# Optimization experiments

Hardware: AMD Instinct MI355X
Metric: run time of the kernel (lower is better)

Reference implementation:

```python
import jax, jax.numpy as jnp
import numpy as np

B, S, D, U = 64, 1024, 512, 512  # batch, seq_len, input dim, lstm units


def setup_inputs() -> dict:
    key = jax.random.key(0)
    ks = jax.random.split(key, 8)
    inputs = jax.random.normal(ks[0], (B, S, D), dtype=jnp.float32)
    # padded speech batch: valid prefix lengths in [S//2, S]
    lengths = jax.random.randint(ks[1], (B,), S // 2, S + 1)
    mask = jnp.arange(S)[None, :] < lengths[:, None]  # [B, S] bool
    s_in, s_rec = 1.0 / np.sqrt(D), 1.0 / np.sqrt(U)
    # Keras LSTM params per direction: kernel [D,4U], recurrent_kernel [U,4U], bias [4U]
    # gate order i, f, g(cell), o ; unit_forget_bias -> forget-gate bias = 1
    bias0 = jnp.zeros((4 * U,), jnp.float32).at[U:2 * U].set(1.0)
    return {
        "inputs": inputs,
        "mask": mask,
        "kernel_f": jax.random.normal(ks[2], (D, 4 * U), jnp.float32) * s_in,
        "rkernel_f": jax.random.normal(ks[3], (U, 4 * U), jnp.float32) * s_rec,
        "bias_f": bias0,
        "kernel_b": jax.random.normal(ks[4], (D, 4 * U), jnp.float32) * s_in,
        "rkernel_b": jax.random.normal(ks[5], (U, 4 * U), jnp.float32) * s_rec,
        "bias_b": bias0,
    }


def _masked_lstm(x, mask, kernel, rkernel, bias):
    """Keras-semantics masked LSTM. x:[B,S,D], mask:[B,S] -> (hs:[B,S,U], h:[B,U], c:[B,U]).
    Masked timesteps carry previous h/c (and emit previous h)."""
    units = rkernel.shape[0]
    # precompute input projection once (big GEMM)
    xz = jnp.einsum('bsd,dk->bsk', x, kernel) + bias  # [B,S,4U]

    def step(carry, inp):
        h, c = carry
        zx, m = inp  # zx:[B,4U], m:[B]
        z = zx + h @ rkernel
        i, f, g, o = jnp.split(z, 4, axis=-1)
        c_new = jax.nn.sigmoid(f) * c + jax.nn.sigmoid(i) * jnp.tanh(g)
        h_new = jax.nn.sigmoid(o) * jnp.tanh(c_new)
        m = m[:, None]
        h = jnp.where(m, h_new, h)
        c = jnp.where(m, c_new, c)
        return (h, c), h

    h0 = jnp.zeros((x.shape[0], units), x.dtype)
    (h, c), hs = jax.lax.scan(step, (h0, h0),
                              (jnp.swapaxes(xz, 0, 1), jnp.swapaxes(mask, 0, 1)))
    return jnp.swapaxes(hs, 0, 1), h, c


def reference(inputs, mask, kernel_f, rkernel_f, bias_f, kernel_b, rkernel_b, bias_b):
    # forward direction
    fwd_out, h_f, c_f = _masked_lstm(inputs, mask, kernel_f, rkernel_f, bias_f)
    # go_backwards=True: Keras reverses inputs AND mask along time
    bwd_out, h_b, c_b = _masked_lstm(inputs[:, ::-1], mask[:, ::-1], kernel_b, rkernel_b, bias_b)
    # wrapper: concat(forward, reverse(backward)) along features
    output = jnp.concatenate([fwd_out, bwd_out[:, ::-1]], axis=-1)  # [B,S,2U]
    return output, h_f, c_f, h_b, c_b
```

## Files before the change

### kernel.cpp

```cpp
#include <hip/hip_runtime.h>

#define S_LEN 1024
#define B_SZ  64
#define D_IN  512
#define U_SZ  512
#define NWG_DIR 64
#define UNITS_PER_WG 8
#define NT 2
#define KSTEPS 32

typedef __attribute__((ext_vector_type(8))) short short8;
typedef __attribute__((ext_vector_type(4))) float floatx4;

union HQ { unsigned long long q[2]; short8 s; };

__device__ __forceinline__ unsigned short f2bf(float f) {
  union { float f; unsigned u; } v; v.f = f;
  unsigned r = v.u + 0x7fffu + ((v.u >> 16) & 1u);
  return (unsigned short)(r >> 16);
}
__device__ __forceinline__ float fsig(float x) {
  return __builtin_amdgcn_rcpf(1.0f + __expf(-x));
}
__device__ __forceinline__ float ftanh(float x) {
  return 1.0f - 2.0f * __builtin_amdgcn_rcpf(__expf(2.0f * x) + 1.0f);
}

__global__ void xprep_kernel(const float* __restrict__ x,
                             unsigned short* __restrict__ Axt) {
  int bs = blockIdx.x;
  int b = bs >> 10, s = bs & 1023;
  float4 v = ((const float4*)x)[(size_t)bs * 128 + threadIdx.x];
  ushort4 o;
  o.x = f2bf(v.x); o.y = f2bf(v.y); o.z = f2bf(v.z); o.w = f2bf(v.w);
  ((ushort4*)(Axt + ((size_t)s * B_SZ + b) * D_IN))[threadIdx.x] = o;
}

__global__ void maskpack_kernel(const unsigned int* __restrict__ mraw,
                                unsigned long long* __restrict__ maskbits) {
  int t = blockIdx.x * blockDim.x + threadIdx.x;
  if (t >= S_LEN) return;
  unsigned d0 = mraw[0];
  unsigned long long bits = 0;
  if (d0 == 1u) {
    const int* m = (const int*)mraw;
    for (int b = 0; b < B_SZ; ++b) if (m[b * S_LEN + t]) bits |= 1ull << b;
  } else if (d0 == 0x3f800000u) {
    const float* m = (const float*)mraw;
    for (int b = 0; b < B_SZ; ++b) if (m[b * S_LEN + t] != 0.f) bits |= 1ull << b;
  } else {
    const unsigned char* m = (const unsigned char*)mraw;
    for (int b = 0; b < B_SZ; ++b) if (m[b * S_LEN + t]) bits |= 1ull << b;
  }
  maskbits[t] = bits;
}

__global__ __launch_bounds__(256, 1) void lstm_scan_kernel(
    const unsigned short* __restrict__ Axt,
    const float* __restrict__ kernel_f, const float* __restrict__ rkernel_f,
    const float* __restrict__ bias_f,
    const float* __restrict__ kernel_b, const float* __restrict__ rkernel_b,
    const float* __restrict__ bias_b,
    const unsigned long long* __restrict__ maskbits,
    unsigned short* __restrict__ hbuf,
    unsigned int* __restrict__ ctrs,
    float* __restrict__ out) {
  __shared__ alignas(16) short lds_b[NT * KSTEPS * 64 * 8];

  const int tid  = threadIdx.x;
  const int lane = tid & 63;
  const int wv   = tid >> 6;
  const int dir  = blockIdx.x >> 6;
  const int wg   = blockIdx.x & 63;
  const int u0   = wg * UNITS_PER_WG;

  const float* Wk   = dir ? kernel_b  : kernel_f;
  const float* Rk   = dir ? rkernel_b : rkernel_f;
  const float* bias = dir ? bias_b    : bias_f;

  for (int item = tid; item < NT * KSTEPS * 64; item += 256) {
    int nt = item >> 11;
    int rem = item & 2047;
    int ks = rem >> 6;
    int ln = rem & 63;
    int kbase = ks * 32 + ((ln >> 4) << 3);
    int col16 = ln & 15;
    int gate = nt * 2 + (col16 >> 3);
    int cg = gate * U_SZ + u0 + (col16 & 7);
    short8 v;
#pragma unroll
    for (int j = 0; j < 8; ++j) {
      int k = kbase + j;
      float f = (k < D_IN) ? Wk[(size_t)k * 2048 + cg]
                           : Rk[(size_t)(k - D_IN) * 2048 + cg];
      v[j] = (short)f2bf(f);
    }
    *(short8*)(&lds_b[item * 8]) = v;
  }
  __syncthreads();

  const int du = lane & 7;
  const int u  = u0 + du;
  float bz[4];
#pragma unroll
  for (int g = 0; g < 4; ++g) bz[g] = bias[g * U_SZ + u];

  float c_st[4] = {0.f, 0.f, 0.f, 0.f};
  float h_st[4] = {0.f, 0.f, 0.f, 0.f};

  unsigned short* hb_base = hbuf + (size_t)dir * 2 * B_SZ * U_SZ;
  unsigned int* ctr = ctrs + dir * 64;

  const int mrow  = lane & 15;
  const int kq    = (lane >> 4) << 3;
  const bool active = (lane & 8) == 0;
  const int brow0 = wv * 16 + ((lane >> 4) << 2);
  const int brow  = wv * 16 + mrow;

  for (int t = 0; t < S_LEN; ++t) {
    const int sx = dir ? (S_LEN - 1 - t) : t;
    const unsigned short* xs =
        Axt + (size_t)sx * B_SZ * D_IN + (size_t)brow * D_IN + kq;
    floatx4 acc0 = {0.f, 0.f, 0.f, 0.f};
    floatx4 acc1 = {0.f, 0.f, 0.f, 0.f};

#pragma unroll
    for (int ks = 0; ks < 16; ++ks) {
      short8 a  = *(const short8*)(xs + ks * 32);
      short8 b0 = *(const short8*)(&lds_b[((0 * KSTEPS + ks) * 64 + lane) * 8]);
      short8 b1 = *(const short8*)(&lds_b[((1 * KSTEPS + ks) * 64 + lane) * 8]);
      acc0 = __builtin_amdgcn_mfma_f32_16x16x32_bf16(a, b0, acc0, 0, 0, 0);
      acc1 = __builtin_amdgcn_mfma_f32_16x16x32_bf16(a, b1, acc1, 0, 0, 0);
    }

    const unsigned long long mb = maskbits[sx];

    if (t > 0) {
      if (tid == 0) {
        unsigned target = (unsigned)(NWG_DIR * t);
        while (__hip_atomic_load(ctr, __ATOMIC_RELAXED,
                                 __HIP_MEMORY_SCOPE_AGENT) < target)
          __builtin_amdgcn_s_sleep(1);
      }
      __syncthreads();
    }

    const unsigned long long* hr = (const unsigned long long*)(
        hb_base + (size_t)((t + 1) & 1) * B_SZ * U_SZ);
    HQ hq[16];
#pragma unroll
    for (int ks = 0; ks < 16; ++ks) {
      int wgp = ks * 4 + (lane >> 4);
      const unsigned long long* p = hr + (size_t)(wgp * 64 + brow) * 2;
      hq[ks].q[0] = __hip_atomic_load(p, __ATOMIC_RELAXED,
                                      __HIP_MEMORY_SCOPE_AGENT);
      hq[ks].q[1] = __hip_atomic_load(p + 1, __ATOMIC_RELAXED,
                                      __HIP_MEMORY_SCOPE_AGENT);
    }
#pragma unroll
    for (int ks = 0; ks < 16; ++ks) {
      short8 b0 = *(const short8*)(&lds_b[((0 * KSTEPS + 16 + ks) * 64 + lane) * 8]);
      short8 b1 = *(const short8*)(&lds_b[((1 * KSTEPS + 16 + ks) * 64 + lane) * 8]);
      acc0 = __builtin_amdgcn_mfma_f32_16x16x32_bf16(hq[ks].s, b0, acc0, 0, 0, 0);
      acc1 = __builtin_amdgcn_mfma_f32_16x16x32_bf16(hq[ks].s, b1, acc1, 0, 0, 0);
    }

#pragma unroll
    for (int r = 0; r < 4; ++r) {
      float iv = acc0[r];
      float gv = acc1[r];
      float fv = __shfl_xor(iv, 8, 64);
      float ov = __shfl_xor(gv, 8, 64);
      float zi = iv + bz[0], zf = fv + bz[1], zg = gv + bz[2], zo = ov + bz[3];
      float cn = fsig(zf) * c_st[r] + fsig(zi) * ftanh(zg);
      float hn = fsig(zo) * ftanh(cn);
      int b = brow0 + r;
      bool m = (mb >> b) & 1ull;
      c_st[r] = m ? cn : c_st[r];
      h_st[r] = m ? hn : h_st[r];
    }

    {
      unsigned short* hw = hb_base + (size_t)(t & 1) * B_SZ * U_SZ +
                           (size_t)wg * 512;
#pragma unroll
      for (int r = 0; r < 4; ++r) {
        unsigned hv = f2bf(h_st[r]);
        unsigned pv = (unsigned)__shfl_xor((int)hv, 1, 64);
        unsigned packed = (hv & 0xffffu) | (pv << 16);
        if (active && !(lane & 1)) {
          int b = brow0 + r;
          __hip_atomic_store((unsigned*)(hw + b * 8 + du), packed,
                             __ATOMIC_RELAXED, __HIP_MEMORY_SCOPE_AGENT);
        }
      }
    }

    asm volatile("s_waitcnt vmcnt(0)" ::: "memory");
    __syncthreads();
    if (tid == 0)
      __hip_atomic_fetch_add(ctr, 1u, __ATOMIC_RELAXED,
                             __HIP_MEMORY_SCOPE_AGENT);

    if (active) {
#pragma unroll
      for (int r = 0; r < 4; ++r) {
        int b = brow0 + r;
        __builtin_nontemporal_store(
            h_st[r], out + ((size_t)b * S_LEN + sx) * 1024 + dir * U_SZ + u);
      }
      if (t == S_LEN - 1) {
        float* fin = out + (size_t)B_SZ * S_LEN * 1024 +
                     (size_t)dir * 2 * B_SZ * U_SZ;
#pragma unroll
        for (int r = 0; r < 4; ++r) {
          int b = brow0 + r;
          fin[b * U_SZ + u] = h_st[r];
          fin[B_SZ * U_SZ + b * U_SZ + u] = c_st[r];
        }
      }
    }
  }
}

extern "C" void kernel_launch(void* const* d_in, const int* in_sizes, int n_in,
                              void* d_out, int out_size, void* d_ws, size_t ws_size,
                              hipStream_t stream) {
  const float* inputs    = (const float*)d_in[0];
  const void*  mask      = d_in[1];
  const float* kernel_f  = (const float*)d_in[2];
  const float* rkernel_f = (const float*)d_in[3];
  const float* bias_f    = (const float*)d_in[4];
  const float* kernel_b  = (const float*)d_in[5];
  const float* rkernel_b = (const float*)d_in[6];
  const float* bias_b    = (const float*)d_in[7];
  float* out = (float*)d_out;

  char* ws = (char*)d_ws;
  unsigned short* Axt = (unsigned short*)ws;
  size_t off = (size_t)S_LEN * B_SZ * D_IN * 2;
  unsigned short* hbuf = (unsigned short*)(ws + off);
  unsigned int* ctrs = (unsigned int*)(ws + off + 262144);
  unsigned long long* maskbits =
      (unsigned long long*)(ws + off + 262144 + 512);

  hipMemsetAsync(hbuf, 0, 262144 + 512, stream);
  maskpack_kernel<<<4, 256, 0, stream>>>((const unsigned int*)mask, maskbits);
  xprep_kernel<<<S_LEN * B_SZ, 128, 0, stream>>>(inputs, Axt);
  lstm_scan_kernel<<<128, 256, 0, stream>>>(Axt, kernel_f, rkernel_f, bias_f,
                                            kernel_b, rkernel_b, bias_b,
                                            maskbits, hbuf, ctrs, out);
}
```

Measured before the change: 6.116 ms.

## Partition LSTM scan by XCD with batch groups and per-slot flag sync

Measured after the change: 4.968 ms. -18.8%, faster.

```diff
diff --git a/kernel.cpp b/kernel.cpp
--- a/kernel.cpp
+++ b/kernel.cpp
@@ -4,15 +4,13 @@
 #define B_SZ  64
 #define D_IN  512
 #define U_SZ  512
-#define NWG_DIR 64
-#define UNITS_PER_WG 8
-#define NT 2
-#define KSTEPS 32
+#define SPIN_CAP (1 << 20)
 
 typedef __attribute__((ext_vector_type(8))) short short8;
 typedef __attribute__((ext_vector_type(4))) float floatx4;
-
-union HQ { unsigned long long q[2]; short8 s; };
+typedef __attribute__((ext_vector_type(4))) unsigned uintx4;
+
+union HU { uintx4 u; short8 s; };
 
 __device__ __forceinline__ unsigned short f2bf(float f) {
   union { float f; unsigned u; } v; v.f = f;
@@ -55,170 +53,184 @@
   maskbits[t] = bits;
 }
 
+__global__ void wprep_kernel(const float* __restrict__ kf,
+                             const float* __restrict__ rf,
+                             const float* __restrict__ kb,
+                             const float* __restrict__ rb,
+                             unsigned short* __restrict__ Wt) {
+  int item = blockIdx.x * 256 + threadIdx.x;
+  int c   = item & 2047;
+  int kc  = (item >> 11) & 255;
+  int dir = item >> 19;
+  const float* K = dir ? kb : kf;
+  const float* R = dir ? rb : rf;
+  int k0 = kc * 4;
+  unsigned long long pk = 0;
+#pragma unroll
+  for (int i = 0; i < 4; ++i) {
+    int k = k0 + i;
+    float f = (k < D_IN) ? K[(size_t)k * 2048 + c]
+                         : R[(size_t)(k - D_IN) * 2048 + c];
+    pk |= (unsigned long long)f2bf(f) << (16 * i);
+  }
+  *(unsigned long long*)(Wt + ((size_t)dir * 2048 + c) * 1024 + k0) = pk;
+}
+
+#define HLOAD(k, boff) \
+  asm volatile("global_load_dwordx4 %0, %1, off offset:" #boff " sc0" \
+               : "=v"(hq[k].u) : "v"(hr))
+
 __global__ __launch_bounds__(256, 1) void lstm_scan_kernel(
     const unsigned short* __restrict__ Axt,
-    const float* __restrict__ kernel_f, const float* __restrict__ rkernel_f,
-    const float* __restrict__ bias_f,
-    const float* __restrict__ kernel_b, const float* __restrict__ rkernel_b,
-    const float* __restrict__ bias_b,
+    const unsigned short* __restrict__ Wt,
+    const float* __restrict__ bias_f, const float* __restrict__ bias_b,
     const unsigned long long* __restrict__ maskbits,
-    unsigned short* __restrict__ hbuf,
-    unsigned int* __restrict__ ctrs,
+    unsigned short* __restrict__ hline,
+    unsigned int* __restrict__ flags,
+    unsigned int* __restrict__ slotctr,
     float* __restrict__ out) {
-  __shared__ alignas(16) short lds_b[NT * KSTEPS * 64 * 8];
+  __shared__ alignas(16) short lds_b[4 * 32 * 64 * 8];
+  __shared__ int sh_xcd, sh_slot;
 
   const int tid  = threadIdx.x;
   const int lane = tid & 63;
   const int wv   = tid >> 6;
-  const int dir  = blockIdx.x >> 6;
-  const int wg   = blockIdx.x & 63;
-  const int u0   = wg * UNITS_PER_WG;
-
-  const float* Wk   = dir ? kernel_b  : kernel_f;
-  const float* Rk   = dir ? rkernel_b : rkernel_f;
-  const float* bias = dir ? bias_b    : bias_f;
-
-  for (int item = tid; item < NT * KSTEPS * 64; item += 256) {
+
+  if (tid == 0) {
+    unsigned x;
+    asm volatile("s_getreg_b32 %0, hwreg(HW_REG_XCC_ID)" : "=s"(x));
+    x &= 7u;
+    sh_xcd  = (int)x;
+    sh_slot = (int)(atomicAdd(&slotctr[x], 1u) & 31u);
+  }
+  __syncthreads();
+  const int xcd  = sh_xcd;
+  const int slot = sh_slot;
+  const int dir  = xcd & 1;
+  const int bg   = xcd >> 1;
+  const int u0   = slot * 16;
+
+  const unsigned short* wsrc = Wt + (size_t)dir * 2048 * 1024;
+  for (int item = tid; item < 4 * 32 * 64; item += 256) {
     int nt = item >> 11;
-    int rem = item & 2047;
-    int ks = rem >> 6;
-    int ln = rem & 63;
+    int ks = (item >> 6) & 31;
+    int ln = item & 63;
+    int cl = nt * 16 + (ln & 15);
+    int Cg = (cl & 3) * U_SZ + u0 + (cl >> 2);
     int kbase = ks * 32 + ((ln >> 4) << 3);
-    int col16 = ln & 15;
-    int gate = nt * 2 + (col16 >> 3);
-    int cg = gate * U_SZ + u0 + (col16 & 7);
-    short8 v;
-#pragma unroll
-    for (int j = 0; j < 8; ++j) {
-      int k = kbase + j;
-      float f = (k < D_IN) ? Wk[(size_t)k * 2048 + cg]
-                           : Rk[(size_t)(k - D_IN) * 2048 + cg];
-      v[j] = (short)f2bf(f);
-    }
+    short8 v = *(const short8*)(wsrc + (size_t)Cg * 1024 + kbase);
     *(short8*)(&lds_b[item * 8]) = v;
   }
   __syncthreads();
 
-  const int du = lane & 7;
-  const int u  = u0 + du;
-  float bz[4];
-#pragma unroll
-  for (int g = 0; g < 4; ++g) bz[g] = bias[g * U_SZ + u];
-
-  float c_st[4] = {0.f, 0.f, 0.f, 0.f};
-  float h_st[4] = {0.f, 0.f, 0.f, 0.f};
-
-  unsigned short* hb_base = hbuf + (size_t)dir * 2 * B_SZ * U_SZ;
-  unsigned int* ctr = ctrs + dir * 64;
-
-  const int mrow  = lane & 15;
-  const int kq    = (lane >> 4) << 3;
-  const bool active = (lane & 8) == 0;
-  const int brow0 = wv * 16 + ((lane >> 4) << 2);
-  const int brow  = wv * 16 + mrow;
+  const int gam = lane & 3;
+  const int du4 = (lane & 15) >> 2;
+  const int u   = u0 + wv * 4 + du4;
+  const int bl  = ((lane >> 4) << 2) + gam;
+  const int bglob = bg * 16 + bl;
+  const float* bias = dir ? bias_b : bias_f;
+  const float bzl = bias[gam * U_SZ + u];
+
+  float c_st = 0.f, h_st = 0.f;
+
+  unsigned short* hgrp = hline + (size_t)xcd * (2 * 16 * 512);
+  unsigned int* fgrp = flags + xcd * 64;
+  const unsigned int* fp = fgrp + (lane & 31);
+
+  const int arow = lane & 15;
+  const int kq   = (lane >> 4) << 3;
 
   for (int t = 0; t < S_LEN; ++t) {
     const int sx = dir ? (S_LEN - 1 - t) : t;
-    const unsigned short* xs =
-        Axt + (size_t)sx * B_SZ * D_IN + (size_t)brow * D_IN + kq;
-    floatx4 acc0 = {0.f, 0.f, 0.f, 0.f};
-    floatx4 acc1 = {0.f, 0.f, 0.f, 0.f};
-
+
+    const unsigned short* xs = Axt + (size_t)sx * B_SZ * D_IN +
+                               (size_t)(bg * 16 + arow) * D_IN + kq;
+    short8 xa[16];
+#pragma unroll
+    for (int ks = 0; ks < 16; ++ks) xa[ks] = *(const short8*)(xs + ks * 32);
+
+    const unsigned long long mb = maskbits[sx];
+
+    floatx4 acc = {0.f, 0.f, 0.f, 0.f};
 #pragma unroll
     for (int ks = 0; ks < 16; ++ks) {
-      short8 a  = *(const short8*)(xs + ks * 32);
-      short8 b0 = *(const short8*)(&lds_b[((0 * KSTEPS + ks) * 64 + lane) * 8]);
-      short8 b1 = *(const short8*)(&lds_b[((1 * KSTEPS + ks) * 64 + lane) * 8]);
-      acc0 = __builtin_amdgcn_mfma_f32_16x16x32_bf16(a, b0, acc0, 0, 0, 0);
-      acc1 = __builtin_amdgcn_mfma_f32_16x16x32_bf16(a, b1, acc1, 0, 0, 0);
-    }
-
-    const unsigned long long mb = maskbits[sx];
+      short8 b = *(const short8*)(&lds_b[((wv * 32 + ks) * 64 + lane) * 8]);
+      acc = __builtin_amdgcn_mfma_f32_16x16x32_bf16(xa[ks], b, acc, 0, 0, 0);
+    }
 
     if (t > 0) {
-      if (tid == 0) {
-        unsigned target = (unsigned)(NWG_DIR * t);
-        while (__hip_atomic_load(ctr, __ATOMIC_RELAXED,
-                                 __HIP_MEMORY_SCOPE_AGENT) < target)
-          __builtin_amdgcn_s_sleep(1);
+      int spins = 0;
+      while (true) {
+        unsigned fv;
+        asm volatile("global_load_dword %0, %1, off sc0\n\t"
+                     "s_waitcnt vmcnt(0)"
+                     : "=v"(fv) : "v"(fp) : "memory");
+        if (__ballot(fv >= (unsigned)t) == ~0ull) break;
+        if (++spins > SPIN_CAP) break;
+        __builtin_amdgcn_s_sleep(1);
       }
-      __syncthreads();
-    }
-
-    const unsigned long long* hr = (const unsigned long long*)(
-        hb_base + (size_t)((t + 1) & 1) * B_SZ * U_SZ);
-    HQ hq[16];
+    }
+
+    const unsigned short* hr = hgrp + (size_t)((t + 1) & 1) * (16 * 512) +
+                               (size_t)arow * 512 + kq;
+    HU hq[16];
+    HLOAD(0, 0);    HLOAD(1, 64);   HLOAD(2, 128);  HLOAD(3, 192);
+    HLOAD(4, 256);  HLOAD(5, 320);  HLOAD(6, 384);  HLOAD(7, 448);
+    HLOAD(8, 512);  HLOAD(9, 576);  HLOAD(10, 640); HLOAD(11, 704);
+    HLOAD(12, 768); HLOAD(13, 832); HLOAD(14, 896); HLOAD(15, 960);
+    asm volatile("s_waitcnt vmcnt(0)" ::: "memory");
+    __builtin_amdgcn_sched_barrier(0);
+
 #pragma unroll
     for (int ks = 0; ks < 16; ++ks) {
-      int wgp = ks * 4 + (lane >> 4);
-      const unsigned long long* p = hr + (size_t)(wgp * 64 + brow) * 2;
-      hq[ks].q[0] = __hip_atomic_load(p, __ATOMIC_RELAXED,
-                                      __HIP_MEMORY_SCOPE_AGENT);
-      hq[ks].q[1] = __hip_atomic_load(p + 1, __ATOMIC_RELAXED,
-                                      __HIP_MEMORY_SCOPE_AGENT);
-    }
-#pragma unroll
-    for (int ks = 0; ks < 16; ++ks) {
-      short8 b0 = *(const short8*)(&lds_b[((0 * KSTEPS + 16 + ks) * 64 + lane) * 8]);
-      short8 b1 = *(const short8*)(&lds_b[((1 * KSTEPS + 16 + ks) * 64 + lane) * 8]);
-      acc0 = __builtin_amdgcn_mfma_f32_16x16x32_bf16(hq[ks].s, b0, acc0, 0, 0, 0);
-      acc1 = __builtin_amdgcn_mfma_f32_16x16x32_bf16(hq[ks].s, b1, acc1, 0, 0, 0);
-    }
-
-#pragma unroll
-    for (int r = 0; r < 4; ++r) {
-      float iv = acc0[r];
-      float gv = acc1[r];
-      float fv = __shfl_xor(iv, 8, 64);
-      float ov = __shfl_xor(gv, 8, 64);
-      float zi = iv + bz[0], zf = fv + bz[1], zg = gv + bz[2], zo = ov + bz[3];
-      float cn = fsig(zf) * c_st[r] + fsig(zi) * ftanh(zg);
-      float hn = fsig(zo) * ftanh(cn);
-      int b = brow0 + r;
-      bool m = (mb >> b) & 1ull;
-      c_st[r] = m ? cn : c_st[r];
-      h_st[r] = m ? hn : h_st[r];
-    }
-
+      short8 b = *(const short8*)(&lds_b[((wv * 32 + 16 + ks) * 64 + lane) * 8]);
+      acc = __builtin_amdgcn_mfma_f32_16x16x32_bf16(hq[ks].s, b, acc, 0, 0, 0);
+    }
+
+    float a0 = acc[0] + bzl, a1 = acc[1] + bzl,
+          a2 = acc[2] + bzl, a3 = acc[3] + bzl;
     {
-      unsigned short* hw = hb_base + (size_t)(t & 1) * B_SZ * U_SZ +
-                           (size_t)wg * 512;
-#pragma unroll
-      for (int r = 0; r < 4; ++r) {
-        unsigned hv = f2bf(h_st[r]);
-        unsigned pv = (unsigned)__shfl_xor((int)hv, 1, 64);
-        unsigned packed = (hv & 0xffffu) | (pv << 16);
-        if (active && !(lane & 1)) {
-          int b = brow0 + r;
-          __hip_atomic_store((unsigned*)(hw + b * 8 + du), packed,
-                             __ATOMIC_RELAXED, __HIP_MEMORY_SCOPE_AGENT);
-        }
-      }
-    }
-
+      float s_, r_;
+      s_ = (gam & 1) ? a0 : a1; r_ = __shfl_xor(s_, 1, 64);
+      if (gam & 1) a0 = r_; else a1 = r_;
+      s_ = (gam & 1) ? a2 : a3; r_ = __shfl_xor(s_, 1, 64);
+      if (gam & 1) a2 = r_; else a3 = r_;
+      s_ = (gam & 2) ? a0 : a2; r_ = __shfl_xor(s_, 2, 64);
+      if (gam & 2) a0 = r_; else a2 = r_;
+      s_ = (gam & 2) ? a1 : a3; r_ = __shfl_xor(s_, 2, 64);
+      if (gam & 2) a1 = r_; else a3 = r_;
+    }
+    {
+      float cn = fsig(a1) * c_st + fsig(a0) * ftanh(a2);
+      float hn = fsig(a3) * ftanh(cn);
+      bool m = (mb >> bglob) & 1ull;
+      c_st = m ? cn : c_st;
+      h_st = m ? hn : h_st;
+    }
+
+    {
+      unsigned short* hw = hgrp + (size_t)(t & 1) * (16 * 512) +
+                           (size_t)bl * 512 + u;
+      unsigned hv = (unsigned)f2bf(h_st);
+      asm volatile("global_store_short %0, %1, off sc0"
+                   :: "v"(hw), "v"(hv) : "memory");
+    }
     asm volatile("s_waitcnt vmcnt(0)" ::: "memory");
     __syncthreads();
-    if (tid == 0)
-      __hip_atomic_fetch_add(ctr, 1u, __ATOMIC_RELAXED,
-                             __HIP_MEMORY_SCOPE_AGENT);
-
-    if (active) {
-#pragma unroll
-      for (int r = 0; r < 4; ++r) {
-        int b = brow0 + r;
-        __builtin_nontemporal_store(
-            h_st[r], out + ((size_t)b * S_LEN + sx) * 1024 + dir * U_SZ + u);
-      }
-      if (t == S_LEN - 1) {
-        float* fin = out + (size_t)B_SZ * S_LEN * 1024 +
-                     (size_t)dir * 2 * B_SZ * U_SZ;
-#pragma unroll
-        for (int r = 0; r < 4; ++r) {
-          int b = brow0 + r;
-          fin[b * U_SZ + u] = h_st[r];
-          fin[B_SZ * U_SZ + b * U_SZ + u] = c_st[r];
-        }
-      }
+    if (tid == 0) {
+      unsigned fv = (unsigned)(t + 1);
+      unsigned int* fs = fgrp + slot;
+      asm volatile("global_store_dword %0, %1, off sc0"
+                   :: "v"(fs), "v"(fv) : "memory");
+    }
+
+    __builtin_nontemporal_store(
+        h_st, out + ((size_t)bglob * S_LEN + sx) * 1024 + dir * U_SZ + u);
+    if (t == S_LEN - 1) {
+      float* fin = out + (size_t)B_SZ * S_LEN * 1024 +
+                   (size_t)dir * 2 * B_SZ * U_SZ;
+      fin[bglob * U_SZ + u] = h_st;
+      fin[B_SZ * U_SZ + bglob * U_SZ + u] = c_st;
     }
   }
 }
@@ -239,15 +251,20 @@
   char* ws = (char*)d_ws;
   unsigned short* Axt = (unsigned short*)ws;
   size_t off = (size_t)S_LEN * B_SZ * D_IN * 2;
-  unsigned short* hbuf = (unsigned short*)(ws + off);
-  unsigned int* ctrs = (unsigned int*)(ws + off + 262144);
+  unsigned short* Wt = (unsigned short*)(ws + off);
+  size_t off2 = off + (size_t)2 * 2048 * 1024 * 2;
+  unsigned short* hline = (unsigned short*)(ws + off2);
+  unsigned int* flags   = (unsigned int*)(ws + off2 + 262144);
+  unsigned int* slotctr = (unsigned int*)(ws + off2 + 262144 + 2048);
   unsigned long long* maskbits =
-      (unsigned long long*)(ws + off + 262144 + 512);
-
-  hipMemsetAsync(hbuf, 0, 262144 + 512, stream);
+      (unsigned long long*)(ws + off2 + 262144 + 2048 + 256);
+
+  hipMemsetAsync(hline, 0, 262144 + 2048 + 256, stream);
   maskpack_kernel<<<4, 256, 0, stream>>>((const unsigned int*)mask, maskbits);
   xprep_kernel<<<S_LEN * B_SZ, 128, 0, stream>>>(inputs, Axt);
-  lstm_scan_kernel<<<128, 256, 0, stream>>>(Axt, kernel_f, rkernel_f, bias_f,
-                                            kernel_b, rkernel_b, bias_b,
-                                            maskbits, hbuf, ctrs, out);
-}
+  wprep_kernel<<<4096, 256, 0, stream>>>(kernel_f, rkernel_f,
+                                         kernel_b, rkernel_b, Wt);
+  lstm_scan_kernel<<<256, 256, 0, stream>>>(Axt, Wt, bias_f, bias_b,
+                                            maskbits, hline, flags, slotctr,
+                                            out);
+}
```
